# Kernel optimization log

Hardware: AMD Instinct MI355X
Metric: run time of the kernel (lower is better)

## Reference

```python
import jax, jax.numpy as jnp
import numpy as np

N = 50000      # nodes
E = 800000     # edges (before self-loops)
F_IN = 128     # num_features
HID = 32       # hidden channels per head (conv1)
HEADS = 4      # conv1 heads
C = 40         # classes (conv2 out channels)
OUT_HEADS = 1  # conv2 heads
NEG_SLOPE = 0.2


def setup_inputs() -> dict:
    key = jax.random.key(0)
    ks = jax.random.split(key, 10)
    x = jax.random.normal(ks[0], (N, F_IN), jnp.float32)
    edge_index = jax.random.randint(ks[1], (2, E), 0, N, jnp.int32)
    s1 = 1.0 / np.sqrt(F_IN).astype(np.float32)
    s1h = 1.0 / np.sqrt(HID).astype(np.float32)
    s2 = 1.0 / np.sqrt(HEADS * HID).astype(np.float32)
    s2c = 1.0 / np.sqrt(C).astype(np.float32)
    W1 = jax.random.normal(ks[2], (F_IN, HEADS * HID), jnp.float32) * s1
    att_src1 = jax.random.normal(ks[3], (HEADS, HID), jnp.float32) * s1h
    att_dst1 = jax.random.normal(ks[4], (HEADS, HID), jnp.float32) * s1h
    bias1 = jnp.zeros((HEADS * HID,), jnp.float32)
    W2 = jax.random.normal(ks[5], (HEADS * HID, OUT_HEADS * C), jnp.float32) * s2
    att_src2 = jax.random.normal(ks[6], (OUT_HEADS, C), jnp.float32) * s2c
    att_dst2 = jax.random.normal(ks[7], (OUT_HEADS, C), jnp.float32) * s2c
    bias2 = jnp.zeros((C,), jnp.float32)
    return {"x": x, "edge_index": edge_index,
            "W1": W1, "att_src1": att_src1, "att_dst1": att_dst1, "bias1": bias1,
            "W2": W2, "att_src2": att_src2, "att_dst2": att_dst2, "bias2": bias2}


def gat_layer(h_in, src, dst, W, a_src, a_dst, bias, heads, out_ch, concat):
    """PyG GATConv (v1) in inference mode (no dropout on attention)."""
    n = h_in.shape[0]
    h = (h_in @ W).reshape(n, heads, out_ch)              # [N,H,F]
    e_src = jnp.einsum('nhf,hf->nh', h, a_src)            # [N,H]
    e_dst = jnp.einsum('nhf,hf->nh', h, a_dst)            # [N,H]
    alpha = jax.nn.leaky_relu(e_src[src] + e_dst[dst], NEG_SLOPE)  # [E,H]
    # segment softmax over destination-node neighborhoods
    amax = jax.ops.segment_max(alpha, dst, num_segments=n)
    amax = jnp.where(jnp.isfinite(amax), amax, 0.0)
    ex = jnp.exp(alpha - amax[dst])
    denom = jax.ops.segment_sum(ex, dst, num_segments=n)
    coef = ex / (denom[dst] + 1e-16)                      # [E,H]
    # scatter-aggregate weighted source messages
    out = jax.ops.segment_sum(h[src] * coef[:, :, None], dst, num_segments=n)  # [N,H,F]
    out = out.reshape(n, heads * out_ch) if concat else out.mean(axis=1)
    return out + bias


def reference(x, edge_index, W1, att_src1, att_dst1, bias1, W2, att_src2, att_dst2, bias2):
    n = x.shape[0]
    loop = jnp.arange(n, dtype=edge_index.dtype)          # GATConv adds self-loops
    src = jnp.concatenate([edge_index[0], loop])
    dst = jnp.concatenate([edge_index[1], loop])
    h = jax.nn.elu(gat_layer(x, src, dst, W1, att_src1, att_dst1, bias1, HEADS, HID, True))
    out = gat_layer(h, src, dst, W2, att_src2, att_dst2, bias2, OUT_HEADS, C, False)
    return (jax.nn.log_softmax(out, axis=1), jax.nn.softmax(out, axis=1))
```

## Files before the change

### kernel.cpp

```cpp
#include <hip/hip_runtime.h>
#include <hip/hip_bf16.h>

#define F1   128
#define H1   4
#define C2   40
#define NEG  0.2f
#define BN   16

typedef __hip_bfloat16 bf16;

__device__ __forceinline__ float ldf(const void* p, size_t i, int isbf) {
    return isbf ? __bfloat162float(((const bf16*)p)[i]) : ((const float*)p)[i];
}
__device__ __forceinline__ float lrelu(float a) { return a > 0.f ? a : NEG * a; }

__device__ __forceinline__ void up2(unsigned g, float& lo, float& hi) {
    lo = __uint_as_float(g << 16);
    hi = __uint_as_float(g & 0xffff0000u);
}

__device__ __forceinline__ void edge_sd(const int* __restrict__ ei, int E, int e,
                                        int& s, int& d) {
    if (e < E) { s = ei[e]; d = ei[E + e]; }
    else       { s = e - E; d = e - E; }
}

__global__ void k_detect(const unsigned short* __restrict__ x, int* __restrict__ flag) {
    __shared__ int sh[256];
    int cnt = 0;
    for (int i = threadIdx.x; i < 8192; i += 256)
        if (((x[i] >> 7) & 0xFF) >= 160) cnt++;
    sh[threadIdx.x] = cnt;
    __syncthreads();
    for (int s = 128; s > 0; s >>= 1) {
        if (threadIdx.x < s) sh[threadIdx.x] += sh[threadIdx.x + s];
        __syncthreads();
    }
    if (threadIdx.x == 0) flag[0] = (sh[0] < 100) ? 1 : 0;
}

__global__ void k_gemm1(const void* __restrict__ x, const void* __restrict__ W1,
                        const void* __restrict__ as1, const void* __restrict__ ad1,
                        const int* __restrict__ flag, const int* __restrict__ ei,
                        int E, int ET, int* __restrict__ deg,
                        bf16* __restrict__ h1b, float* __restrict__ es1,
                        float* __restrict__ ed1, int N) {
    int per = (ET + gridDim.x - 1) / gridDim.x;
    int he0 = blockIdx.x * per;
    int he1 = he0 + per; if (he1 > ET) he1 = ET;
    for (int e = he0 + threadIdx.x; e < he1; e += 256) {
        int d = (e < E) ? ei[E + e] : e - E;
        atomicAdd(&deg[d], 1);
    }
    __shared__ float xs[BN][F1];
    const int isbf = flag[0];
    int n0 = blockIdx.x * BN, t = threadIdx.x;
    for (int i = t; i < BN * F1; i += 256) {
        int nn = i >> 7, kk = i & 127;
        int n = n0 + nn; if (n >= N) n = N - 1;
        xs[nn][kk] = ldf(x, (size_t)n * F1 + kk, isbf);
    }
    __syncthreads();
    int col = t & 127, nh = t >> 7;
    float a[8] = {0.f, 0.f, 0.f, 0.f, 0.f, 0.f, 0.f, 0.f};
    if (isbf) {
        const bf16* W = (const bf16*)W1;
#pragma unroll 4
        for (int k = 0; k < F1; k++) {
            float w = __bfloat162float(W[(size_t)k * F1 + col]);
#pragma unroll
            for (int j = 0; j < 8; j++) a[j] = fmaf(xs[nh + 2 * j][k], w, a[j]);
        }
    } else {
        const float* W = (const float*)W1;
#pragma unroll 4
        for (int k = 0; k < F1; k++) {
            float w = W[(size_t)k * F1 + col];
#pragma unroll
            for (int j = 0; j < 8; j++) a[j] = fmaf(xs[nh + 2 * j][k], w, a[j]);
        }
    }
    float asv = ldf(as1, col, isbf), adv = ldf(ad1, col, isbf);
    int h = col >> 5;
#pragma unroll
    for (int j = 0; j < 8; j++) {
        int n = n0 + nh + 2 * j;
        float s = a[j] * asv, dd = a[j] * adv;
#pragma unroll
        for (int off = 16; off > 0; off >>= 1) {
            s += __shfl_down(s, off, 32);
            dd += __shfl_down(dd, off, 32);
        }
        if (n < N) {
            h1b[(size_t)n * F1 + col] = __float2bfloat16(a[j]);
            if ((t & 31) == 0) { es1[n * H1 + h] = s; ed1[n * H1 + h] = dd; }
        }
    }
}

__global__ void k_scan1(const int* __restrict__ deg, int N, int* __restrict__ part) {
    __shared__ int sh[256];
    int i = blockIdx.x * 256 + threadIdx.x;
    sh[threadIdx.x] = (i < N) ? deg[i] : 0;
    __syncthreads();
    for (int s = 128; s > 0; s >>= 1) {
        if (threadIdx.x < s) sh[threadIdx.x] += sh[threadIdx.x + s];
        __syncthreads();
    }
    if (threadIdx.x == 0) part[blockIdx.x] = sh[0];
}

__global__ void k_scan2(int* __restrict__ part, int NB) {
    __shared__ int sh[256];
    int t = threadIdx.x;
    int v = (t < NB) ? part[t] : 0;
    sh[t] = v;
    __syncthreads();
    for (int off = 1; off < 256; off <<= 1) {
        int add = (t >= off) ? sh[t - off] : 0;
        __syncthreads();
        sh[t] += add;
        __syncthreads();
    }
    if (t < NB) part[t] = sh[t] - v;
}

__global__ void k_scan3(const int* __restrict__ deg, int N, const int* __restrict__ part,
                        int* __restrict__ offs) {
    __shared__ int sh[256];
    int t = threadIdx.x, i = blockIdx.x * 256 + t;
    int v = (i < N) ? deg[i] : 0;
    sh[t] = v;
    __syncthreads();
    for (int off = 1; off < 256; off <<= 1) {
        int add = (t >= off) ? sh[t - off] : 0;
        __syncthreads();
        sh[t] += add;
        __syncthreads();
    }
    if (i < N) offs[i] = sh[t] - v + part[blockIdx.x];
}

__global__ void k_scatter(const int* __restrict__ ei, int E, int ET,
                          int* __restrict__ offs, int* __restrict__ ebuf) {
    int e = blockIdx.x * blockDim.x + threadIdx.x;
    if (e >= ET) return;
    int s, d; edge_sd(ei, E, e, s, d);
    int pos = atomicAdd(&offs[d], 1);
    ebuf[pos] = s;
}

__global__ void __launch_bounds__(256) k_l1(
        const int* __restrict__ offs, const int* __restrict__ ebuf,
        const float* __restrict__ es1, const float* __restrict__ ed1,
        const uint4* __restrict__ h1p4, const void* __restrict__ b1,
        const void* __restrict__ W2, const void* __restrict__ as2,
        const void* __restrict__ ad2, const int* __restrict__ flag,
        bf16* __restrict__ h2b, float* __restrict__ es2, float* __restrict__ ed2,
        int N) {
    int w = threadIdx.x >> 6, l = threadIdx.x & 63;
    int d = blockIdx.x * 4 + w; if (d >= N) d = N - 1;
    int start = d ? offs[d - 1] : 0, end = offs[d];
    int q = l >> 4, c16 = l & 15, h = c16 >> 2;
    float edh = ed1[d * H1 + h];
    float acc[8] = {0.f, 0.f, 0.f, 0.f, 0.f, 0.f, 0.f, 0.f};
    float dsum = 0.f;

    auto body = [&](int base) {
        int e_i = base + q;
        int s = ebuf[e_i];
        float esv = es1[s * H1 + h];
        uint4 g = h1p4[(size_t)s * 16 + c16];
        float ev = __expf(lrelu(esv + edh));
        float lo, hi;
        up2(g.x, lo, hi); acc[0] = fmaf(ev, lo, acc[0]); acc[1] = fmaf(ev, hi, acc[1]);
        up2(g.y, lo, hi); acc[2] = fmaf(ev, lo, acc[2]); acc[3] = fmaf(ev, hi, acc[3]);
        up2(g.z, lo, hi); acc[4] = fmaf(ev, lo, acc[4]); acc[5] = fmaf(ev, hi, acc[5]);
        up2(g.w, lo, hi); acc[6] = fmaf(ev, lo, acc[6]); acc[7] = fmaf(ev, hi, acc[7]);
        dsum += ev;
    };

    int i = start;
    for (; i + 8 <= end; i += 8) { body(i); body(i + 4); }
    for (; i + 4 <= end; i += 4) body(i);
    if (i < end && i + q < end) body(i);

#pragma unroll
    for (int off = 16; off <= 32; off <<= 1) {
#pragma unroll
        for (int j = 0; j < 8; j++) acc[j] += __shfl_xor(acc[j], off, 64);
        dsum += __shfl_xor(dsum, off, 64);
    }

    const int isbf = flag[0];
    __shared__ float hs[4][F1];
    if (q == 0) {
        float inv = 1.f / (dsum + 1e-16f);
#pragma unroll
        for (int j = 0; j < 8; j++) {
            int col = c16 * 8 + j;
            float v = acc[j] * inv + ldf(b1, col, isbf);
            hs[w][col] = v > 0.f ? v : (__expf(v) - 1.f);
        }
    }
    __syncthreads();
    float a2 = 0.f;
    if (l < C2) {
        if (isbf) {
            const bf16* W = (const bf16*)W2;
#pragma unroll 8
            for (int k = 0; k < F1; k++)
                a2 = fmaf(hs[w][k], __bfloat162float(W[(size_t)k * C2 + l]), a2);
        } else {
            const float* W = (const float*)W2;
#pragma unroll 8
            for (int k = 0; k < F1; k++) a2 = fmaf(hs[w][k], W[(size_t)k * C2 + l], a2);
        }
        h2b[(size_t)d * C2 + l] = __float2bfloat16(a2);
    }
    float ps = (l < C2) ? a2 * ldf(as2, l, isbf) : 0.f;
    float pd = (l < C2) ? a2 * ldf(ad2, l, isbf) : 0.f;
#pragma unroll
    for (int off = 32; off > 0; off >>= 1) {
        ps += __shfl_xor(ps, off, 64);
        pd += __shfl_xor(pd, off, 64);
    }
    if (l == 0) { es2[d] = ps; ed2[d] = pd; }
}

__global__ void __launch_bounds__(256) k_l2(
        const int* __restrict__ offs, const int* __restrict__ ebuf,
        const float* __restrict__ es2, const float* __restrict__ ed2,
        const unsigned* __restrict__ h2p, const void* __restrict__ b2,
        const int* __restrict__ flag, void* __restrict__ out, int N) {
    int w = threadIdx.x >> 6, l = threadIdx.x & 63;
    int d = blockIdx.x * 4 + w; if (d >= N) d = N - 1;
    int start = d ? offs[d - 1] : 0, end = offs[d];
    float edd = ed2[d];
    int half = l >> 5, j = l & 31;
    float acc0 = 0.f, acc1 = 0.f, dsum = 0.f;

    auto proc1 = [&](int e) {
        int s = ebuf[e];
        float xv = __expf(lrelu(es2[s] + edd));
        if (j < 20) {
            float lo, hi; up2(h2p[(size_t)s * 20 + j], lo, hi);
            acc0 = fmaf(xv, lo, acc0); acc1 = fmaf(xv, hi, acc1);
        }
        dsum += xv;
    };

    int i = start;
    for (; i + 8 <= end; i += 8) {
        int b = i + half * 4;
        int s0 = ebuf[b], s1 = ebuf[b + 1], s2 = ebuf[b + 2], s3 = ebuf[b + 3];
        float x0 = __expf(lrelu(es2[s0] + edd));
        float x1 = __expf(lrelu(es2[s1] + edd));
        float x2 = __expf(lrelu(es2[s2] + edd));
        float x3 = __expf(lrelu(es2[s3] + edd));
        if (j < 20) {
            unsigned g0 = h2p[(size_t)s0 * 20 + j], g1 = h2p[(size_t)s1 * 20 + j];
            unsigned g2 = h2p[(size_t)s2 * 20 + j], g3 = h2p[(size_t)s3 * 20 + j];
            float lo, hi;
            up2(g0, lo, hi); acc0 = fmaf(x0, lo, acc0); acc1 = fmaf(x0, hi, acc1);
            up2(g1, lo, hi); acc0 = fmaf(x1, lo, acc0); acc1 = fmaf(x1, hi, acc1);
            up2(g2, lo, hi); acc0 = fmaf(x2, lo, acc0); acc1 = fmaf(x2, hi, acc1);
            up2(g3, lo, hi); acc0 = fmaf(x3, lo, acc0); acc1 = fmaf(x3, hi, acc1);
        }
        dsum += (x0 + x1) + (x2 + x3);
    }
    for (; i + 2 <= end; i += 2) proc1(i + half);
    if (i < end && half == 0) proc1(i);

    acc0 += __shfl_xor(acc0, 32, 64);
    acc1 += __shfl_xor(acc1, 32, 64);
    dsum += __shfl_xor(dsum, 32, 64);

    const int isbf = flag[0];
    float inv = 1.f / (dsum + 1e-16f);
    float v0 = -1e30f, v1 = -1e30f;
    if (l < 20) {
        v0 = acc0 * inv + ldf(b2, 2 * l, isbf);
        v1 = acc1 * inv + ldf(b2, 2 * l + 1, isbf);
    }
    float m = fmaxf(v0, v1);
#pragma unroll
    for (int off = 16; off > 0; off >>= 1) m = fmaxf(m, __shfl_xor(m, off, 32));
    float sv = (l < 20) ? __expf(v0 - m) + __expf(v1 - m) : 0.f;
#pragma unroll
    for (int off = 16; off > 0; off >>= 1) sv += __shfl_xor(sv, off, 32);
    float lse = m + __logf(sv);
    if (l < 20) {
        float ls0 = v0 - lse, ls1 = v1 - lse;
        size_t base = (size_t)d * C2 + 2 * l, halfo = (size_t)N * C2;
        if (isbf) {
            bf16* o = (bf16*)out;
            o[base] = __float2bfloat16(ls0);
            o[base + 1] = __float2bfloat16(ls1);
            o[halfo + base] = __float2bfloat16(__expf(ls0));
            o[halfo + base + 1] = __float2bfloat16(__expf(ls1));
        } else {
            float* o = (float*)out;
            o[base] = ls0;
            o[base + 1] = ls1;
            o[halfo + base] = __expf(ls0);
            o[halfo + base + 1] = __expf(ls1);
        }
    }
}

extern "C" void kernel_launch(void* const* d_in, const int* in_sizes, int n_in,
                              void* d_out, int out_size, void* d_ws, size_t ws_size,
                              hipStream_t stream) {
    const int N  = in_sizes[0] / F1;
    const int E  = in_sizes[1] / 2;
    const int ET = E + N;
    const int NB = (N + 255) / 256;

    const void* x   = d_in[0];
    const int*  ei  = (const int*)d_in[1];
    const void* W1  = d_in[2];
    const void* as1 = d_in[3];
    const void* ad1 = d_in[4];
    const void* b1  = d_in[5];
    const void* W2  = d_in[6];
    const void* as2 = d_in[7];
    const void* ad2 = d_in[8];
    const void* b2  = d_in[9];

    float* ws = (float*)d_ws;
    auto al4 = [](size_t v) { return (v + 3) & ~(size_t)3; };
    size_t o = 0;
    bf16*  h1b  = (bf16*)(ws + o); o = al4(o + (size_t)64 * N);
    float* es1  = ws + o; o = al4(o + (size_t)H1 * N);
    float* ed1  = ws + o; o = al4(o + (size_t)H1 * N);
    bf16*  h2b  = (bf16*)(ws + o); o = al4(o + (size_t)20 * N);
    float* es2  = ws + o; o = al4(o + N);
    float* ed2  = ws + o; o = al4(o + N);
    int*   deg  = (int*)(ws + o); o = al4(o + N);
    int*   offs = (int*)(ws + o); o = al4(o + N);
    int*   part = (int*)(ws + o); o = al4(o + 256);
    int*   flag = (int*)(ws + o); o = al4(o + 4);
    int*   ebuf = (int*)(ws + o); o = al4(o + ET);

    const int T = 256;
    k_detect<<<1, 256, 0, stream>>>((const unsigned short*)x, flag);
    hipMemsetAsync(deg, 0, (size_t)N * sizeof(int), stream);

    k_gemm1<<<(N + BN - 1) / BN, 256, 0, stream>>>(x, W1, as1, ad1, flag, ei, E, ET,
                                                   deg, h1b, es1, ed1, N);
    k_scan1<<<NB, 256, 0, stream>>>(deg, N, part);
    k_scan2<<<1, 256, 0, stream>>>(part, NB);
    k_scan3<<<NB, 256, 0, stream>>>(deg, N, part, offs);
    k_scatter<<<(ET + T - 1) / T, T, 0, stream>>>(ei, E, ET, offs, ebuf);
    k_l1<<<(N + 3) / 4, 256, 0, stream>>>(offs, ebuf, es1, ed1, (const uint4*)h1b,
                                          b1, W2, as2, ad2, flag, h2b, es2, ed2, N);
    k_l2<<<(N + 3) / 4, 256, 0, stream>>>(offs, ebuf, es2, ed2, (const unsigned*)h2b,
                                          b2, flag, d_out, N);
}
```

Before: 345.1 us.

## Use fp16 dot2 in layer-1 GEMM, stage W2 in LDS, unroll edge loop

The first-layer projection now packs x and W1 into fp16 pairs in shared memory and accumulates with the packed fdot2 instruction, which halves the inner-loop iterations and LDS reads. The layer-1 aggregation kernel stages W2 in shared memory so the per-node second GEMM reads from LDS instead of global memory, and its edge gather loop is unrolled to 16 edges per iteration. The cost is fp16 rounding of the inputs and weights, each block reloading all of W1 and W2 into LDS, and higher register and LDS use that may lower occupancy.

```diff
diff --git a/kernel.cpp b/kernel.cpp
--- a/kernel.cpp
+++ b/kernel.cpp
@@ -8,6 +8,7 @@
 #define BN   16
 
 typedef __hip_bfloat16 bf16;
+typedef _Float16 hf2 __attribute__((ext_vector_type(2)));
 
 __device__ __forceinline__ float ldf(const void* p, size_t i, int isbf) {
     return isbf ? __bfloat162float(((const bf16*)p)[i]) : ((const float*)p)[i];
@@ -17,6 +18,20 @@
 __device__ __forceinline__ void up2(unsigned g, float& lo, float& hi) {
     lo = __uint_as_float(g << 16);
     hi = __uint_as_float(g & 0xffff0000u);
+}
+
+__device__ __forceinline__ unsigned pack2(float a, float b) {
+    hf2 p; p[0] = (_Float16)a; p[1] = (_Float16)b;
+    return __builtin_bit_cast(unsigned, p);
+}
+__device__ __forceinline__ float dot2(unsigned a, unsigned b, float c) {
+#if __has_builtin(__builtin_amdgcn_fdot2)
+    return __builtin_amdgcn_fdot2(__builtin_bit_cast(hf2, a),
+                                  __builtin_bit_cast(hf2, b), c, false);
+#else
+    hf2 x = __builtin_bit_cast(hf2, a), y = __builtin_bit_cast(hf2, b);
+    return c + (float)x[0] * (float)y[0] + (float)x[1] * (float)y[1];
+#endif
 }
 
 __device__ __forceinline__ void edge_sd(const int* __restrict__ ei, int E, int e,
@@ -39,47 +54,50 @@
     if (threadIdx.x == 0) flag[0] = (sh[0] < 100) ? 1 : 0;
 }
 
-__global__ void k_gemm1(const void* __restrict__ x, const void* __restrict__ W1,
-                        const void* __restrict__ as1, const void* __restrict__ ad1,
-                        const int* __restrict__ flag, const int* __restrict__ ei,
-                        int E, int ET, int* __restrict__ deg,
-                        bf16* __restrict__ h1b, float* __restrict__ es1,
-                        float* __restrict__ ed1, int N) {
+__global__ void __launch_bounds__(256) k_gemm1(
+        const void* __restrict__ x, const void* __restrict__ W1,
+        const void* __restrict__ as1, const void* __restrict__ ad1,
+        const int* __restrict__ flag, const int* __restrict__ ei,
+        int E, int ET, int* __restrict__ deg,
+        bf16* __restrict__ h1b, float* __restrict__ es1,
+        float* __restrict__ ed1, int N) {
+    __shared__ unsigned wp[64][F1];
+    __shared__ unsigned xh[BN][64];
+    const int isbf = flag[0];
+    int t = threadIdx.x, n0 = blockIdx.x * BN;
+
     int per = (ET + gridDim.x - 1) / gridDim.x;
     int he0 = blockIdx.x * per;
     int he1 = he0 + per; if (he1 > ET) he1 = ET;
-    for (int e = he0 + threadIdx.x; e < he1; e += 256) {
+    for (int e = he0 + t; e < he1; e += 256) {
         int d = (e < E) ? ei[E + e] : e - E;
         atomicAdd(&deg[d], 1);
     }
-    __shared__ float xs[BN][F1];
-    const int isbf = flag[0];
-    int n0 = blockIdx.x * BN, t = threadIdx.x;
-    for (int i = t; i < BN * F1; i += 256) {
-        int nn = i >> 7, kk = i & 127;
+
+    for (int i = t; i < 64 * F1; i += 256) {
+        int m = i >> 7, c = i & 127;
+        float w0 = ldf(W1, (size_t)(2 * m) * F1 + c, isbf);
+        float w1 = ldf(W1, (size_t)(2 * m + 1) * F1 + c, isbf);
+        wp[m][c] = pack2(w0, w1);
+    }
+    for (int i = t; i < BN * 64; i += 256) {
+        int nn = i >> 6, m = i & 63;
         int n = n0 + nn; if (n >= N) n = N - 1;
-        xs[nn][kk] = ldf(x, (size_t)n * F1 + kk, isbf);
-    }
-    __syncthreads();
+        float x0 = ldf(x, (size_t)n * F1 + 2 * m, isbf);
+        float x1 = ldf(x, (size_t)n * F1 + 2 * m + 1, isbf);
+        xh[nn][m] = pack2(x0, x1);
+    }
+    __syncthreads();
+
     int col = t & 127, nh = t >> 7;
     float a[8] = {0.f, 0.f, 0.f, 0.f, 0.f, 0.f, 0.f, 0.f};
-    if (isbf) {
-        const bf16* W = (const bf16*)W1;
 #pragma unroll 4
-        for (int k = 0; k < F1; k++) {
-            float w = __bfloat162float(W[(size_t)k * F1 + col]);
-#pragma unroll
-            for (int j = 0; j < 8; j++) a[j] = fmaf(xs[nh + 2 * j][k], w, a[j]);
-        }
-    } else {
-        const float* W = (const float*)W1;
-#pragma unroll 4
-        for (int k = 0; k < F1; k++) {
-            float w = W[(size_t)k * F1 + col];
-#pragma unroll
-            for (int j = 0; j < 8; j++) a[j] = fmaf(xs[nh + 2 * j][k], w, a[j]);
-        }
-    }
+    for (int m = 0; m < 64; m++) {
+        unsigned w = wp[m][col];
+#pragma unroll
+        for (int j = 0; j < 8; j++) a[j] = dot2(xh[nh + 2 * j][m], w, a[j]);
+    }
+
     float asv = ldf(as1, col, isbf), adv = ldf(ad1, col, isbf);
     int h = col >> 5;
 #pragma unroll
@@ -158,7 +176,12 @@
         const void* __restrict__ ad2, const int* __restrict__ flag,
         bf16* __restrict__ h2b, float* __restrict__ es2, float* __restrict__ ed2,
         int N) {
-    int w = threadIdx.x >> 6, l = threadIdx.x & 63;
+    __shared__ float w2s[F1][C2];
+    __shared__ float hs[4][F1];
+    const int isbf = flag[0];
+    int w = threadIdx.x >> 6, l = threadIdx.x & 63, t = threadIdx.x;
+    for (int i = t; i < F1 * C2; i += 256) w2s[i / C2][i % C2] = ldf(W2, i, isbf);
+
     int d = blockIdx.x * 4 + w; if (d >= N) d = N - 1;
     int start = d ? offs[d - 1] : 0, end = offs[d];
     int q = l >> 4, c16 = l & 15, h = c16 >> 2;
@@ -181,7 +204,7 @@
     };
 
     int i = start;
-    for (; i + 8 <= end; i += 8) { body(i); body(i + 4); }
+    for (; i + 16 <= end; i += 16) { body(i); body(i + 4); body(i + 8); body(i + 12); }
     for (; i + 4 <= end; i += 4) body(i);
     if (i < end && i + q < end) body(i);
 
@@ -192,8 +215,6 @@
         dsum += __shfl_xor(dsum, off, 64);
     }
 
-    const int isbf = flag[0];
-    __shared__ float hs[4][F1];
     if (q == 0) {
         float inv = 1.f / (dsum + 1e-16f);
 #pragma unroll
@@ -206,16 +227,8 @@
     __syncthreads();
     float a2 = 0.f;
     if (l < C2) {
-        if (isbf) {
-            const bf16* W = (const bf16*)W2;
 #pragma unroll 8
-            for (int k = 0; k < F1; k++)
-                a2 = fmaf(hs[w][k], __bfloat162float(W[(size_t)k * C2 + l]), a2);
-        } else {
-            const float* W = (const float*)W2;
-#pragma unroll 8
-            for (int k = 0; k < F1; k++) a2 = fmaf(hs[w][k], W[(size_t)k * C2 + l], a2);
-        }
+        for (int k = 0; k < F1; k++) a2 = fmaf(hs[w][k], w2s[k][l], a2);
         h2b[(size_t)d * C2 + l] = __float2bfloat16(a2);
     }
     float ps = (l < C2) ? a2 * ldf(as2, l, isbf) : 0.f;
```

Result: slower. 374.2 us (+8.4%).

## Pad layer-2 features to 48 and gather 16-byte vectors per edge

Applied to the files above, without the earlier changes.

Pads the layer-2 hidden rows from 40 to 48 bf16 so each row is six 16-byte chunks. k_l2 now handles 8 edges at once per wavefront, 8 lanes per edge, with each of 5 active lanes loading a uint4 instead of one 32-bit word. The epilogue softmax is reorganised to match. Both aggregation kernels switch to packed f32x2 accumulators so the compiler can emit packed FMA. The aim is fewer, wider gather loads and more edges in flight, at the cost of 20% padding in h2 storage and 3 of 8 lanes idle per edge group.

```diff
diff --git a/kernel.cpp b/kernel.cpp
--- a/kernel.cpp
+++ b/kernel.cpp
@@ -6,17 +6,21 @@
 #define C2   40
 #define NEG  0.2f
 #define BN   16
+#define H2S  48
 
 typedef __hip_bfloat16 bf16;
+typedef float f32x2 __attribute__((ext_vector_type(2)));
 
 __device__ __forceinline__ float ldf(const void* p, size_t i, int isbf) {
     return isbf ? __bfloat162float(((const bf16*)p)[i]) : ((const float*)p)[i];
 }
 __device__ __forceinline__ float lrelu(float a) { return a > 0.f ? a : NEG * a; }
 
-__device__ __forceinline__ void up2(unsigned g, float& lo, float& hi) {
-    lo = __uint_as_float(g << 16);
-    hi = __uint_as_float(g & 0xffff0000u);
+__device__ __forceinline__ f32x2 up2v(unsigned g) {
+    f32x2 r;
+    r.x = __uint_as_float(g << 16);
+    r.y = __uint_as_float(g & 0xffff0000u);
+    return r;
 }
 
 __device__ __forceinline__ void edge_sd(const int* __restrict__ ei, int E, int e,
@@ -163,7 +167,7 @@
     int start = d ? offs[d - 1] : 0, end = offs[d];
     int q = l >> 4, c16 = l & 15, h = c16 >> 2;
     float edh = ed1[d * H1 + h];
-    float acc[8] = {0.f, 0.f, 0.f, 0.f, 0.f, 0.f, 0.f, 0.f};
+    f32x2 acc[4] = {{0.f, 0.f}, {0.f, 0.f}, {0.f, 0.f}, {0.f, 0.f}};
     float dsum = 0.f;
 
     auto body = [&](int base) {
@@ -172,11 +176,11 @@
         float esv = es1[s * H1 + h];
         uint4 g = h1p4[(size_t)s * 16 + c16];
         float ev = __expf(lrelu(esv + edh));
-        float lo, hi;
-        up2(g.x, lo, hi); acc[0] = fmaf(ev, lo, acc[0]); acc[1] = fmaf(ev, hi, acc[1]);
-        up2(g.y, lo, hi); acc[2] = fmaf(ev, lo, acc[2]); acc[3] = fmaf(ev, hi, acc[3]);
-        up2(g.z, lo, hi); acc[4] = fmaf(ev, lo, acc[4]); acc[5] = fmaf(ev, hi, acc[5]);
-        up2(g.w, lo, hi); acc[6] = fmaf(ev, lo, acc[6]); acc[7] = fmaf(ev, hi, acc[7]);
+        f32x2 ev2 = {ev, ev};
+        acc[0] += ev2 * up2v(g.x);
+        acc[1] += ev2 * up2v(g.y);
+        acc[2] += ev2 * up2v(g.z);
+        acc[3] += ev2 * up2v(g.w);
         dsum += ev;
     };
 
@@ -188,7 +192,10 @@
 #pragma unroll
     for (int off = 16; off <= 32; off <<= 1) {
 #pragma unroll
-        for (int j = 0; j < 8; j++) acc[j] += __shfl_xor(acc[j], off, 64);
+        for (int j = 0; j < 4; j++) {
+            acc[j].x += __shfl_xor(acc[j].x, off, 64);
+            acc[j].y += __shfl_xor(acc[j].y, off, 64);
+        }
         dsum += __shfl_xor(dsum, off, 64);
     }
 
@@ -199,7 +206,8 @@
 #pragma unroll
         for (int j = 0; j < 8; j++) {
             int col = c16 * 8 + j;
-            float v = acc[j] * inv + ldf(b1, col, isbf);
+            float av = (j & 1) ? acc[j >> 1].y : acc[j >> 1].x;
+            float v = av * inv + ldf(b1, col, isbf);
             hs[w][col] = v > 0.f ? v : (__expf(v) - 1.f);
         }
     }
@@ -216,7 +224,7 @@
 #pragma unroll 8
             for (int k = 0; k < F1; k++) a2 = fmaf(hs[w][k], W[(size_t)k * C2 + l], a2);
         }
-        h2b[(size_t)d * C2 + l] = __float2bfloat16(a2);
+        h2b[(size_t)d * H2S + l] = __float2bfloat16(a2);
     }
     float ps = (l < C2) ? a2 * ldf(as2, l, isbf) : 0.f;
     float pd = (l < C2) ? a2 * ldf(ad2, l, isbf) : 0.f;
@@ -231,80 +239,74 @@
 __global__ void __launch_bounds__(256) k_l2(
         const int* __restrict__ offs, const int* __restrict__ ebuf,
         const float* __restrict__ es2, const float* __restrict__ ed2,
-        const unsigned* __restrict__ h2p, const void* __restrict__ b2,
+        const uint4* __restrict__ h2p4, const void* __restrict__ b2,
         const int* __restrict__ flag, void* __restrict__ out, int N) {
     int w = threadIdx.x >> 6, l = threadIdx.x & 63;
     int d = blockIdx.x * 4 + w; if (d >= N) d = N - 1;
     int start = d ? offs[d - 1] : 0, end = offs[d];
     float edd = ed2[d];
-    int half = l >> 5, j = l & 31;
-    float acc0 = 0.f, acc1 = 0.f, dsum = 0.f;
-
-    auto proc1 = [&](int e) {
+    int g8 = l >> 3, j8 = l & 7;
+    f32x2 acc[4] = {{0.f, 0.f}, {0.f, 0.f}, {0.f, 0.f}, {0.f, 0.f}};
+    float dsum = 0.f;
+
+    auto body = [&](int e) {
         int s = ebuf[e];
         float xv = __expf(lrelu(es2[s] + edd));
-        if (j < 20) {
-            float lo, hi; up2(h2p[(size_t)s * 20 + j], lo, hi);
-            acc0 = fmaf(xv, lo, acc0); acc1 = fmaf(xv, hi, acc1);
+        if (j8 < 5) {
+            uint4 g = h2p4[(size_t)s * 6 + j8];
+            f32x2 xv2 = {xv, xv};
+            acc[0] += xv2 * up2v(g.x);
+            acc[1] += xv2 * up2v(g.y);
+            acc[2] += xv2 * up2v(g.z);
+            acc[3] += xv2 * up2v(g.w);
         }
         dsum += xv;
     };
 
     int i = start;
-    for (; i + 8 <= end; i += 8) {
-        int b = i + half * 4;
-        int s0 = ebuf[b], s1 = ebuf[b + 1], s2 = ebuf[b + 2], s3 = ebuf[b + 3];
-        float x0 = __expf(lrelu(es2[s0] + edd));
-        float x1 = __expf(lrelu(es2[s1] + edd));
-        float x2 = __expf(lrelu(es2[s2] + edd));
-        float x3 = __expf(lrelu(es2[s3] + edd));
-        if (j < 20) {
-            unsigned g0 = h2p[(size_t)s0 * 20 + j], g1 = h2p[(size_t)s1 * 20 + j];
-            unsigned g2 = h2p[(size_t)s2 * 20 + j], g3 = h2p[(size_t)s3 * 20 + j];
-            float lo, hi;
-            up2(g0, lo, hi); acc0 = fmaf(x0, lo, acc0); acc1 = fmaf(x0, hi, acc1);
-            up2(g1, lo, hi); acc0 = fmaf(x1, lo, acc0); acc1 = fmaf(x1, hi, acc1);
-            up2(g2, lo, hi); acc0 = fmaf(x2, lo, acc0); acc1 = fmaf(x2, hi, acc1);
-            up2(g3, lo, hi); acc0 = fmaf(x3, lo, acc0); acc1 = fmaf(x3, hi, acc1);
-        }
-        dsum += (x0 + x1) + (x2 + x3);
-    }
-    for (; i + 2 <= end; i += 2) proc1(i + half);
-    if (i < end && half == 0) proc1(i);
-
-    acc0 += __shfl_xor(acc0, 32, 64);
-    acc1 += __shfl_xor(acc1, 32, 64);
-    dsum += __shfl_xor(dsum, 32, 64);
+    for (; i + 8 <= end; i += 8) body(i + g8);
+    if (i + g8 < end) body(i + g8);
+
+#pragma unroll
+    for (int off = 8; off <= 32; off <<= 1) {
+#pragma unroll
+        for (int j = 0; j < 4; j++) {
+            acc[j].x += __shfl_xor(acc[j].x, off, 64);
+            acc[j].y += __shfl_xor(acc[j].y, off, 64);
+        }
+        dsum += __shfl_xor(dsum, off, 64);
+    }
 
     const int isbf = flag[0];
     float inv = 1.f / (dsum + 1e-16f);
-    float v0 = -1e30f, v1 = -1e30f;
-    if (l < 20) {
-        v0 = acc0 * inv + ldf(b2, 2 * l, isbf);
-        v1 = acc1 * inv + ldf(b2, 2 * l + 1, isbf);
-    }
-    float m = fmaxf(v0, v1);
-#pragma unroll
-    for (int off = 16; off > 0; off >>= 1) m = fmaxf(m, __shfl_xor(m, off, 32));
-    float sv = (l < 20) ? __expf(v0 - m) + __expf(v1 - m) : 0.f;
-#pragma unroll
-    for (int off = 16; off > 0; off >>= 1) sv += __shfl_xor(sv, off, 32);
-    float lse = m + __logf(sv);
-    if (l < 20) {
-        float ls0 = v0 - lse, ls1 = v1 - lse;
-        size_t base = (size_t)d * C2 + 2 * l, halfo = (size_t)N * C2;
-        if (isbf) {
-            bf16* o = (bf16*)out;
-            o[base] = __float2bfloat16(ls0);
-            o[base + 1] = __float2bfloat16(ls1);
-            o[halfo + base] = __float2bfloat16(__expf(ls0));
-            o[halfo + base + 1] = __float2bfloat16(__expf(ls1));
-        } else {
-            float* o = (float*)out;
-            o[base] = ls0;
-            o[base + 1] = ls1;
-            o[halfo + base] = __expf(ls0);
-            o[halfo + base + 1] = __expf(ls1);
+    float v[8], m = -1e30f;
+#pragma unroll
+    for (int k = 0; k < 8; k++) {
+        int c = 8 * j8 + k;
+        float av = (k & 1) ? acc[k >> 1].y : acc[k >> 1].x;
+        v[k] = (c < C2) ? av * inv + ldf(b2, c, isbf) : -1e30f;
+        m = fmaxf(m, v[k]);
+    }
+#pragma unroll
+    for (int off = 1; off <= 4; off <<= 1) m = fmaxf(m, __shfl_xor(m, off, 64));
+    float se = 0.f;
+#pragma unroll
+    for (int k = 0; k < 8; k++) se += (8 * j8 + k < C2) ? __expf(v[k] - m) : 0.f;
+#pragma unroll
+    for (int off = 1; off <= 4; off <<= 1) se += __shfl_xor(se, off, 64);
+    float lse = m + __logf(se);
+    if (g8 == 0 && j8 < 5) {
+        size_t base = (size_t)d * C2 + 8 * j8, halfo = (size_t)N * C2;
+#pragma unroll
+        for (int k = 0; k < 8; k++) {
+            float ls = v[k] - lse, sm = __expf(ls);
+            if (isbf) {
+                ((bf16*)out)[base + k] = __float2bfloat16(ls);
+                ((bf16*)out)[halfo + base + k] = __float2bfloat16(sm);
+            } else {
+                ((float*)out)[base + k] = ls;
+                ((float*)out)[halfo + base + k] = sm;
+            }
         }
     }
 }
@@ -334,7 +336,7 @@
     bf16*  h1b  = (bf16*)(ws + o); o = al4(o + (size_t)64 * N);
     float* es1  = ws + o; o = al4(o + (size_t)H1 * N);
     float* ed1  = ws + o; o = al4(o + (size_t)H1 * N);
-    bf16*  h2b  = (bf16*)(ws + o); o = al4(o + (size_t)20 * N);
+    bf16*  h2b  = (bf16*)(ws + o); o = al4(o + (size_t)24 * N);
     float* es2  = ws + o; o = al4(o + N);
     float* ed2  = ws + o; o = al4(o + N);
     int*   deg  = (int*)(ws + o); o = al4(o + N);
@@ -355,6 +357,6 @@
     k_scatter<<<(ET + T - 1) / T, T, 0, stream>>>(ei, E, ET, offs, ebuf);
     k_l1<<<(N + 3) / 4, 256, 0, stream>>>(offs, ebuf, es1, ed1, (const uint4*)h1b,
                                           b1, W2, as2, ad2, flag, h2b, es2, ed2, N);
-    k_l2<<<(N + 3) / 4, 256, 0, stream>>>(offs, ebuf, es2, ed2, (const unsigned*)h2b,
+    k_l2<<<(N + 3) / 4, 256, 0, stream>>>(offs, ebuf, es2, ed2, (const uint4*)h2b,
                                           b2, flag, d_out, N);
 }
```

After: 355.8 us. 3.1% more time.

## Pad degree/offset counters to separate cache lines; vectorize layer-1 accumulation

Applied to the files above, without the earlier changes.

Spreads the per-node degree and offset counters to a stride of 32 ints (128 bytes), so that atomics from different destinations hit different cache lines and contend less. The layer-1 aggregation now accumulates into float2 vectors, which allows packed FMA, and its edge loop is unrolled by 12 instead of 8. The cost is a 32x larger memset and counter footprint (about 6.4 MB each), plus strided, uncoalesced reads in the scan and aggregation kernels.

```diff
diff --git a/kernel.cpp b/kernel.cpp
--- a/kernel.cpp
+++ b/kernel.cpp
@@ -6,8 +6,10 @@
 #define C2   40
 #define NEG  0.2f
 #define BN   16
+#define CP   32
 
 typedef __hip_bfloat16 bf16;
+typedef float f32x2 __attribute__((ext_vector_type(2)));
 
 __device__ __forceinline__ float ldf(const void* p, size_t i, int isbf) {
     return isbf ? __bfloat162float(((const bf16*)p)[i]) : ((const float*)p)[i];
@@ -17,6 +19,12 @@
 __device__ __forceinline__ void up2(unsigned g, float& lo, float& hi) {
     lo = __uint_as_float(g << 16);
     hi = __uint_as_float(g & 0xffff0000u);
+}
+__device__ __forceinline__ f32x2 up2v(unsigned g) {
+    f32x2 r;
+    r.x = __uint_as_float(g << 16);
+    r.y = __uint_as_float(g & 0xffff0000u);
+    return r;
 }
 
 __device__ __forceinline__ void edge_sd(const int* __restrict__ ei, int E, int e,
@@ -50,7 +58,7 @@
     int he1 = he0 + per; if (he1 > ET) he1 = ET;
     for (int e = he0 + threadIdx.x; e < he1; e += 256) {
         int d = (e < E) ? ei[E + e] : e - E;
-        atomicAdd(&deg[d], 1);
+        atomicAdd(&deg[(size_t)d * CP], 1);
     }
     __shared__ float xs[BN][F1];
     const int isbf = flag[0];
@@ -101,7 +109,7 @@
 __global__ void k_scan1(const int* __restrict__ deg, int N, int* __restrict__ part) {
     __shared__ int sh[256];
     int i = blockIdx.x * 256 + threadIdx.x;
-    sh[threadIdx.x] = (i < N) ? deg[i] : 0;
+    sh[threadIdx.x] = (i < N) ? deg[(size_t)i * CP] : 0;
     __syncthreads();
     for (int s = 128; s > 0; s >>= 1) {
         if (threadIdx.x < s) sh[threadIdx.x] += sh[threadIdx.x + s];
@@ -129,7 +137,7 @@
                         int* __restrict__ offs) {
     __shared__ int sh[256];
     int t = threadIdx.x, i = blockIdx.x * 256 + t;
-    int v = (i < N) ? deg[i] : 0;
+    int v = (i < N) ? deg[(size_t)i * CP] : 0;
     sh[t] = v;
     __syncthreads();
     for (int off = 1; off < 256; off <<= 1) {
@@ -138,7 +146,7 @@
         sh[t] += add;
         __syncthreads();
     }
-    if (i < N) offs[i] = sh[t] - v + part[blockIdx.x];
+    if (i < N) offs[(size_t)i * CP] = sh[t] - v + part[blockIdx.x];
 }
 
 __global__ void k_scatter(const int* __restrict__ ei, int E, int ET,
@@ -146,7 +154,7 @@
     int e = blockIdx.x * blockDim.x + threadIdx.x;
     if (e >= ET) return;
     int s, d; edge_sd(ei, E, e, s, d);
-    int pos = atomicAdd(&offs[d], 1);
+    int pos = atomicAdd(&offs[(size_t)d * CP], 1);
     ebuf[pos] = s;
 }
 
@@ -160,10 +168,11 @@
         int N) {
     int w = threadIdx.x >> 6, l = threadIdx.x & 63;
     int d = blockIdx.x * 4 + w; if (d >= N) d = N - 1;
-    int start = d ? offs[d - 1] : 0, end = offs[d];
+    int start = d ? offs[(size_t)(d - 1) * CP] : 0;
+    int end = offs[(size_t)d * CP];
     int q = l >> 4, c16 = l & 15, h = c16 >> 2;
     float edh = ed1[d * H1 + h];
-    float acc[8] = {0.f, 0.f, 0.f, 0.f, 0.f, 0.f, 0.f, 0.f};
+    f32x2 acc[4] = {{0.f, 0.f}, {0.f, 0.f}, {0.f, 0.f}, {0.f, 0.f}};
     float dsum = 0.f;
 
     auto body = [&](int base) {
@@ -172,23 +181,26 @@
         float esv = es1[s * H1 + h];
         uint4 g = h1p4[(size_t)s * 16 + c16];
         float ev = __expf(lrelu(esv + edh));
-        float lo, hi;
-        up2(g.x, lo, hi); acc[0] = fmaf(ev, lo, acc[0]); acc[1] = fmaf(ev, hi, acc[1]);
-        up2(g.y, lo, hi); acc[2] = fmaf(ev, lo, acc[2]); acc[3] = fmaf(ev, hi, acc[3]);
-        up2(g.z, lo, hi); acc[4] = fmaf(ev, lo, acc[4]); acc[5] = fmaf(ev, hi, acc[5]);
-        up2(g.w, lo, hi); acc[6] = fmaf(ev, lo, acc[6]); acc[7] = fmaf(ev, hi, acc[7]);
+        f32x2 ev2 = {ev, ev};
+        acc[0] += ev2 * up2v(g.x);
+        acc[1] += ev2 * up2v(g.y);
+        acc[2] += ev2 * up2v(g.z);
+        acc[3] += ev2 * up2v(g.w);
         dsum += ev;
     };
 
     int i = start;
-    for (; i + 8 <= end; i += 8) { body(i); body(i + 4); }
+    for (; i + 12 <= end; i += 12) { body(i); body(i + 4); body(i + 8); }
     for (; i + 4 <= end; i += 4) body(i);
     if (i < end && i + q < end) body(i);
 
 #pragma unroll
     for (int off = 16; off <= 32; off <<= 1) {
 #pragma unroll
-        for (int j = 0; j < 8; j++) acc[j] += __shfl_xor(acc[j], off, 64);
+        for (int j = 0; j < 4; j++) {
+            acc[j].x += __shfl_xor(acc[j].x, off, 64);
+            acc[j].y += __shfl_xor(acc[j].y, off, 64);
+        }
         dsum += __shfl_xor(dsum, off, 64);
     }
 
@@ -199,7 +211,8 @@
 #pragma unroll
         for (int j = 0; j < 8; j++) {
             int col = c16 * 8 + j;
-            float v = acc[j] * inv + ldf(b1, col, isbf);
+            float av = (j & 1) ? acc[j >> 1].y : acc[j >> 1].x;
+            float v = av * inv + ldf(b1, col, isbf);
             hs[w][col] = v > 0.f ? v : (__expf(v) - 1.f);
         }
     }
@@ -235,7 +248,8 @@
         const int* __restrict__ flag, void* __restrict__ out, int N) {
     int w = threadIdx.x >> 6, l = threadIdx.x & 63;
     int d = blockIdx.x * 4 + w; if (d >= N) d = N - 1;
-    int start = d ? offs[d - 1] : 0, end = offs[d];
+    int start = d ? offs[(size_t)(d - 1) * CP] : 0;
+    int end = offs[(size_t)d * CP];
     float edd = ed2[d];
     int half = l >> 5, j = l & 31;
     float acc0 = 0.f, acc1 = 0.f, dsum = 0.f;
@@ -337,15 +351,15 @@
     bf16*  h2b  = (bf16*)(ws + o); o = al4(o + (size_t)20 * N);
     float* es2  = ws + o; o = al4(o + N);
     float* ed2  = ws + o; o = al4(o + N);
-    int*   deg  = (int*)(ws + o); o = al4(o + N);
-    int*   offs = (int*)(ws + o); o = al4(o + N);
+    int*   deg  = (int*)(ws + o); o = al4(o + (size_t)CP * N);
+    int*   offs = (int*)(ws + o); o = al4(o + (size_t)CP * N);
     int*   part = (int*)(ws + o); o = al4(o + 256);
     int*   flag = (int*)(ws + o); o = al4(o + 4);
     int*   ebuf = (int*)(ws + o); o = al4(o + ET);
 
     const int T = 256;
     k_detect<<<1, 256, 0, stream>>>((const unsigned short*)x, flag);
-    hipMemsetAsync(deg, 0, (size_t)N * sizeof(int), stream);
+    hipMemsetAsync(deg, 0, (size_t)CP * N * sizeof(int), stream);
 
     k_gemm1<<<(N + BN - 1) / BN, 256, 0, stream>>>(x, W1, as1, ad1, flag, ei, E, ET,
                                                    deg, h1b, es1, ed1, N);
```

Result: slower. 354.8 us (+2.8%).
